# Optimization experiments

Hardware: AMD Instinct MI355X
Metric: run time of the kernel (lower is better)

The kernel has to match this reference:

```python
import jax, jax.numpy as jnp
import numpy as np

DROP_SPLITS = 2
KERNEL = 3


def setup_inputs() -> dict:
    key = jax.random.key(0)
    k1, k2, k3 = jax.random.split(key, 3)
    B, C, H, W = 32, 128, 128, 128
    Cin = C - C // DROP_SPLITS  # actual_in_channels = 64
    Cout = 128
    x = jax.random.normal(k1, (B, C, H, W), dtype=jnp.float32)
    w = jax.random.normal(k2, (Cout, Cin, KERNEL, KERNEL), dtype=jnp.float32) * 0.05
    b = jax.random.normal(k3, (Cout,), dtype=jnp.float32) * 0.05
    return {"x": x, "w": w, "b": b}


def reference(x, w, b):
    # x: [B, C, H, W]; w: [Cout, Cin, K, K]; b: [Cout]
    Cin = w.shape[1]
    ch_sum = x.sum(axis=(-2, -1))                 # [B, C] per-channel spatial sums
    idx = jnp.argsort(ch_sum, axis=1)[:, :Cin]    # [B, Cin] lowest-sum channels
    # batched gather of selected channels (replaces per-sample python loop)
    sel = jnp.take_along_axis(x, idx[:, :, None, None], axis=1)  # [B, Cin, H, W]
    pad = KERNEL // 2
    out = jax.lax.conv_general_dilated(
        sel, w,
        window_strides=(1, 1),
        padding=[(pad, pad), (pad, pad)],
        dimension_numbers=("NCHW", "OIHW", "NCHW"),
    )
    return out + b[None, :, None, None]
```

## Files before the change

### kernel.cpp

```cpp
#include <hip/hip_runtime.h>

#define B_ 32
#define C_ 128
#define HW_ 128
#define CIN_ 64
#define COUT_ 128
#define SPATIAL (HW_ * HW_)

typedef unsigned short u16;
typedef unsigned int u32;
typedef short s16x8 __attribute__((ext_vector_type(8)));
typedef float f32x16 __attribute__((ext_vector_type(16)));

__device__ __forceinline__ void split_bf16(float x, u16& hi, u16& lo) {
    u32 u = __float_as_uint(x);
    u32 rh = (u + 0x7FFFu + ((u >> 16) & 1u)) >> 16;
    float hf = __uint_as_float(rh << 16);
    float r = x - hf;
    u32 v = __float_as_uint(r);
    u32 rl = (v + 0x7FFFu + ((v >> 16) & 1u)) >> 16;
    hi = (u16)rh; lo = (u16)rl;
}

__device__ __forceinline__ u16 rnd_bf16(float x) {
    u32 u = __float_as_uint(x);
    return (u16)((u + 0x7FFFu + ((u >> 16) & 1u)) >> 16);
}

__global__ __launch_bounds__(256) void k_chansum(const float* __restrict__ x,
                                                 double* __restrict__ sums) {
    int bc = blockIdx.x;
    const float4* p4 = (const float4*)(x + (size_t)bc * SPATIAL);
    int t = threadIdx.x;
    double s = 0.0;
#pragma unroll
    for (int i = 0; i < 16; ++i) {
        float4 v = p4[t + 256 * i];
        s += (double)v.x + (double)v.y + (double)v.z + (double)v.w;
    }
#pragma unroll
    for (int off = 32; off > 0; off >>= 1) s += __shfl_down(s, off, 64);
    __shared__ double wsum[4];
    if ((t & 63) == 0) wsum[t >> 6] = s;
    __syncthreads();
    if (t == 0) sums[bc] = wsum[0] + wsum[1] + wsum[2] + wsum[3];
}

__global__ __launch_bounds__(128) void k_select(const double* __restrict__ sums,
                                                int* __restrict__ idx) {
    int b = blockIdx.x, c = threadIdx.x;
    __shared__ double s[C_];
    double my = sums[b * C_ + c];
    s[c] = my;
    __syncthreads();
    int rank = 0;
    for (int j = 0; j < C_; ++j) {
        double v = s[j];
        rank += (v < my || (v == my && j < c)) ? 1 : 0;
    }
    if (rank < CIN_) idx[b * CIN_ + rank] = c;
}

__global__ __launch_bounds__(256) void k_wprep(const float* __restrict__ w,
                                               u16* __restrict__ wf) {
    int bid = blockIdx.x;
    int hl = bid / 144, rem = bid % 144;
    int tap = rem / 16, r2 = rem % 16;
    int ks = r2 / 4, cot = r2 % 4;
    int dh = tap / 3, dw = tap % 3;
    for (int j = threadIdx.x; j < 512; j += 256) {
        int lane = j >> 3, e = j & 7;
        int co = cot * 32 + (lane & 31);
        int ci = ks * 16 + (lane >> 5) * 8 + e;
        float v = w[((co * CIN_ + ci) * 3 + dh) * 3 + dw];
        u16 h, l; split_bf16(v, h, l);
        wf[(size_t)bid * 512 + j] = hl ? l : h;
    }
}

#define ROWS 8
#define WC 32

__global__ __launch_bounds__(256, 2) void k_conv_mfma(
    const float* __restrict__ x, const u16* __restrict__ wf,
    const float* __restrict__ bias, const int* __restrict__ idx,
    float* __restrict__ out)
{
    __shared__ __align__(16) u16 tH[10 * 34 * 32];
    __shared__ int sidx[CIN_];

    const int b = blockIdx.z;
    const int h0 = blockIdx.y * ROWS;
    const int w0 = blockIdx.x * WC;
    const int t = threadIdx.x;
    const int lane = t & 63;
    const int wv = t >> 6;
    const int g  = wv & 1;
    const int rg = wv >> 1;
    const int lc = lane & 31;
    const int lk = lane >> 5;

    if (t < CIN_) sidx[t] = idx[b * CIN_ + t];

    f32x16 acc[2][4];
#pragma unroll
    for (int ct = 0; ct < 2; ++ct)
#pragma unroll
        for (int q = 0; q < 16; ++q) {
            int row = (q & 3) + 8 * (q >> 2) + 4 * lk;
            float bv = bias[g * 64 + ct * 32 + row];
#pragma unroll
            for (int rr = 0; rr < 4; ++rr) acc[ct][rr][q] = bv;
        }

    const float* xb = x + ((size_t)b << 21);

    for (int ch = 0; ch < 2; ++ch) {
        __syncthreads();
        for (int e = t; e < 4 * 10 * 34; e += 256) {
            int w_  = e % 34;
            int tmp = e / 34;
            int r   = tmp % 10;
            int s   = tmp / 10;
            int gh = h0 + r - 1, gw = w0 + w_ - 1;
            bool ok = ((unsigned)gh < (unsigned)HW_) && ((unsigned)gw < (unsigned)HW_);
            int cb = ch * 32 + s * 8;
            uint4 ph = {0, 0, 0, 0};
            if (ok) {
                int off = (gh << 7) + gw;
                float v0 = xb[((size_t)sidx[cb + 0] << 14) + off];
                float v1 = xb[((size_t)sidx[cb + 1] << 14) + off];
                float v2 = xb[((size_t)sidx[cb + 2] << 14) + off];
                float v3 = xb[((size_t)sidx[cb + 3] << 14) + off];
                float v4 = xb[((size_t)sidx[cb + 4] << 14) + off];
                float v5 = xb[((size_t)sidx[cb + 5] << 14) + off];
                float v6 = xb[((size_t)sidx[cb + 6] << 14) + off];
                float v7 = xb[((size_t)sidx[cb + 7] << 14) + off];
                ph.x = (u32)rnd_bf16(v0) | ((u32)rnd_bf16(v1) << 16);
                ph.y = (u32)rnd_bf16(v2) | ((u32)rnd_bf16(v3) << 16);
                ph.z = (u32)rnd_bf16(v4) | ((u32)rnd_bf16(v5) << 16);
                ph.w = (u32)rnd_bf16(v6) | ((u32)rnd_bf16(v7) << 16);
            }
            int slot = s ^ ((w_ >> 1) & 3);
            int si = (r * 34 + w_) * 32 + slot * 8;
            *(uint4*)&tH[si] = ph;
        }
        __syncthreads();

#pragma unroll 1
        for (int dh = 0; dh < 3; ++dh) {
#pragma unroll
            for (int dw = 0; dw < 3; ++dw) {
                int tap = dh * 3 + dw;
                int wT = lc + dw;
                int rbase = (rg * 4 + dh) * 34 + wT;
#pragma unroll
                for (int kci = 0; kci < 2; ++kci) {
                    int sw = ((kci * 2 + lk) ^ ((wT >> 1) & 3)) * 8;
                    uint4 bh[4];
#pragma unroll
                    for (int rr = 0; rr < 4; ++rr) {
                        int a = (rbase + rr * 34) * 32 + sw;
                        bh[rr] = *(const uint4*)&tH[a];
                    }
                    int ks = ch * 2 + kci;
                    const u16* pH = wf + ((size_t)(((0 * 9 + tap) * 4 + ks) * 4 + g * 2) * 64 + lane) * 8;
                    const u16* pL = wf + ((size_t)(((1 * 9 + tap) * 4 + ks) * 4 + g * 2) * 64 + lane) * 8;
#pragma unroll
                    for (int ct = 0; ct < 2; ++ct) {
                        s16x8 ah = *(const s16x8*)(pH + ct * 512);
                        s16x8 al = *(const s16x8*)(pL + ct * 512);
#pragma unroll
                        for (int rr = 0; rr < 4; ++rr) {
                            s16x8 bhv = __builtin_bit_cast(s16x8, bh[rr]);
                            acc[ct][rr] = __builtin_amdgcn_mfma_f32_32x32x16_bf16(ah, bhv, acc[ct][rr], 0, 0, 0);
                            acc[ct][rr] = __builtin_amdgcn_mfma_f32_32x32x16_bf16(al, bhv, acc[ct][rr], 0, 0, 0);
                        }
                    }
                }
            }
        }
    }

    const int orow0 = h0 + rg * 4;
    size_t ob = (((size_t)(b * COUT_ + g * 64)) << 14) + ((size_t)orow0 << 7) + w0 + lc;
#pragma unroll
    for (int ct = 0; ct < 2; ++ct)
#pragma unroll
        for (int rr = 0; rr < 4; ++rr)
#pragma unroll
            for (int q = 0; q < 16; ++q) {
                int row = (q & 3) + 8 * (q >> 2) + 4 * lk;
                out[ob + (((size_t)(ct * 32 + row)) << 14) + ((size_t)rr << 7)] = acc[ct][rr][q];
            }
}

extern "C" void kernel_launch(void* const* d_in, const int* in_sizes, int n_in,
                              void* d_out, int out_size, void* d_ws, size_t ws_size,
                              hipStream_t stream) {
    const float* x    = (const float*)d_in[0];
    const float* w    = (const float*)d_in[1];
    const float* bias = (const float*)d_in[2];
    float* out = (float*)d_out;

    double* sums = (double*)d_ws;
    int* idx     = (int*)((char*)d_ws + 32768);
    u16* wfrag   = (u16*)((char*)d_ws + 40960);

    k_chansum<<<B_ * C_, 256, 0, stream>>>(x, sums);
    k_select<<<B_, 128, 0, stream>>>(sums, idx);
    k_wprep<<<288, 256, 0, stream>>>(w, wfrag);

    dim3 grid(HW_ / WC, HW_ / ROWS, B_);
    k_conv_mfma<<<grid, 256, 0, stream>>>(x, wfrag, bias, idx, out);
}
```

Baseline: 607.8 us.

## Double-buffer 16-channel input tiles with register prefetch overlapping MFMA compute

Splits the 64 selected input channels into four 16-channel stages with two LDS buffers. The global gathers for the next stage are held in registers while MFMAs run on the current buffer, then written to LDS after a barrier. This hides global load latency behind compute, and the MFMA block also raises wave priority with s_setprio. The cost is 24 extra prefetch registers per thread on top of the large accumulator set, which may hurt occupancy or cause spills, plus more barriers.

```diff
diff --git a/kernel.cpp b/kernel.cpp
--- a/kernel.cpp
+++ b/kernel.cpp
@@ -25,6 +25,10 @@
 __device__ __forceinline__ u16 rnd_bf16(float x) {
     u32 u = __float_as_uint(x);
     return (u16)((u + 0x7FFFu + ((u >> 16) & 1u)) >> 16);
+}
+
+__device__ __forceinline__ u32 pack2(float a, float b) {
+    return (u32)rnd_bf16(a) | ((u32)rnd_bf16(b) << 16);
 }
 
 __global__ __launch_bounds__(256) void k_chansum(const float* __restrict__ x,
@@ -80,13 +84,15 @@
 
 #define ROWS 8
 #define WC 32
+#define TSZ (10 * 34 * 16)
+#define UNITS (2 * 10 * 34)
 
 __global__ __launch_bounds__(256, 2) void k_conv_mfma(
     const float* __restrict__ x, const u16* __restrict__ wf,
     const float* __restrict__ bias, const int* __restrict__ idx,
     float* __restrict__ out)
 {
-    __shared__ __align__(16) u16 tH[10 * 34 * 32];
+    __shared__ __align__(16) u16 tile[2][TSZ];
     __shared__ int sidx[CIN_];
 
     const int b = blockIdx.z;
@@ -115,70 +121,97 @@
 
     const float* xb = x + ((size_t)b << 21);
 
-    for (int ch = 0; ch < 2; ++ch) {
-        __syncthreads();
-        for (int e = t; e < 4 * 10 * 34; e += 256) {
+    float pre[3][8];
+
+    auto issue = [&](int qq) {
+#pragma unroll
+        for (int u = 0; u < 3; ++u) {
+            int e = t + 256 * u;
+            bool ve = (e < UNITS);
             int w_  = e % 34;
             int tmp = e / 34;
             int r   = tmp % 10;
             int s   = tmp / 10;
             int gh = h0 + r - 1, gw = w0 + w_ - 1;
-            bool ok = ((unsigned)gh < (unsigned)HW_) && ((unsigned)gw < (unsigned)HW_);
-            int cb = ch * 32 + s * 8;
-            uint4 ph = {0, 0, 0, 0};
-            if (ok) {
-                int off = (gh << 7) + gw;
-                float v0 = xb[((size_t)sidx[cb + 0] << 14) + off];
-                float v1 = xb[((size_t)sidx[cb + 1] << 14) + off];
-                float v2 = xb[((size_t)sidx[cb + 2] << 14) + off];
-                float v3 = xb[((size_t)sidx[cb + 3] << 14) + off];
-                float v4 = xb[((size_t)sidx[cb + 4] << 14) + off];
-                float v5 = xb[((size_t)sidx[cb + 5] << 14) + off];
-                float v6 = xb[((size_t)sidx[cb + 6] << 14) + off];
-                float v7 = xb[((size_t)sidx[cb + 7] << 14) + off];
-                ph.x = (u32)rnd_bf16(v0) | ((u32)rnd_bf16(v1) << 16);
-                ph.y = (u32)rnd_bf16(v2) | ((u32)rnd_bf16(v3) << 16);
-                ph.z = (u32)rnd_bf16(v4) | ((u32)rnd_bf16(v5) << 16);
-                ph.w = (u32)rnd_bf16(v6) | ((u32)rnd_bf16(v7) << 16);
-            }
-            int slot = s ^ ((w_ >> 1) & 3);
-            int si = (r * 34 + w_) * 32 + slot * 8;
-            *(uint4*)&tH[si] = ph;
-        }
-        __syncthreads();
-
-#pragma unroll 1
+            bool ok = ve && ((unsigned)gh < (unsigned)HW_) && ((unsigned)gw < (unsigned)HW_);
+            int off = (gh << 7) + gw;
+            int cb = qq * 16 + s * 8;
+#pragma unroll
+            for (int i = 0; i < 8; ++i) {
+                float v = 0.f;
+                if (ok) v = xb[((size_t)sidx[cb + i] << 14) + off];
+                pre[u][i] = v;
+            }
+        }
+    };
+
+    auto commit = [&](int buf) {
+#pragma unroll
+        for (int u = 0; u < 3; ++u) {
+            int e = t + 256 * u;
+            if (e < UNITS) {
+                int w_  = e % 34;
+                int tmp = e / 34;
+                int r   = tmp % 10;
+                int s   = tmp / 10;
+                uint4 ph;
+                ph.x = pack2(pre[u][0], pre[u][1]);
+                ph.y = pack2(pre[u][2], pre[u][3]);
+                ph.z = pack2(pre[u][4], pre[u][5]);
+                ph.w = pack2(pre[u][6], pre[u][7]);
+                int slot = s ^ ((w_ >> 2) & 1);
+                int si = (r * 34 + w_) * 16 + slot * 8;
+                *(uint4*)&tile[buf][si] = ph;
+            }
+        }
+    };
+
+    auto compute = [&](int qq, int buf) {
+#pragma unroll
         for (int dh = 0; dh < 3; ++dh) {
 #pragma unroll
             for (int dw = 0; dw < 3; ++dw) {
-                int tap = dh * 3 + dw;
+                const int tap = dh * 3 + dw;
                 int wT = lc + dw;
-                int rbase = (rg * 4 + dh) * 34 + wT;
-#pragma unroll
-                for (int kci = 0; kci < 2; ++kci) {
-                    int sw = ((kci * 2 + lk) ^ ((wT >> 1) & 3)) * 8;
-                    uint4 bh[4];
+                int sr = (lk ^ ((wT >> 2) & 1)) * 8;
+                uint4 bh[4];
+#pragma unroll
+                for (int rr = 0; rr < 4; ++rr) {
+                    int a = ((rg * 4 + dh + rr) * 34 + wT) * 16 + sr;
+                    bh[rr] = *(const uint4*)&tile[buf][a];
+                }
+                const u16* pH = wf + ((size_t)(((0 * 9 + tap) * 4 + qq) * 4 + g * 2) << 9) + lane * 8;
+                const u16* pL = wf + ((size_t)(((1 * 9 + tap) * 4 + qq) * 4 + g * 2) << 9) + lane * 8;
+                __builtin_amdgcn_s_setprio(1);
+#pragma unroll
+                for (int ct = 0; ct < 2; ++ct) {
+                    s16x8 ah = *(const s16x8*)(pH + ct * 512);
+                    s16x8 al = *(const s16x8*)(pL + ct * 512);
 #pragma unroll
                     for (int rr = 0; rr < 4; ++rr) {
-                        int a = (rbase + rr * 34) * 32 + sw;
-                        bh[rr] = *(const uint4*)&tH[a];
-                    }
-                    int ks = ch * 2 + kci;
-                    const u16* pH = wf + ((size_t)(((0 * 9 + tap) * 4 + ks) * 4 + g * 2) * 64 + lane) * 8;
-                    const u16* pL = wf + ((size_t)(((1 * 9 + tap) * 4 + ks) * 4 + g * 2) * 64 + lane) * 8;
-#pragma unroll
-                    for (int ct = 0; ct < 2; ++ct) {
-                        s16x8 ah = *(const s16x8*)(pH + ct * 512);
-                        s16x8 al = *(const s16x8*)(pL + ct * 512);
-#pragma unroll
-                        for (int rr = 0; rr < 4; ++rr) {
-                            s16x8 bhv = __builtin_bit_cast(s16x8, bh[rr]);
-                            acc[ct][rr] = __builtin_amdgcn_mfma_f32_32x32x16_bf16(ah, bhv, acc[ct][rr], 0, 0, 0);
-                            acc[ct][rr] = __builtin_amdgcn_mfma_f32_32x32x16_bf16(al, bhv, acc[ct][rr], 0, 0, 0);
-                        }
+                        s16x8 bv = __builtin_bit_cast(s16x8, bh[rr]);
+                        acc[ct][rr] = __builtin_amdgcn_mfma_f32_32x32x16_bf16(ah, bv, acc[ct][rr], 0, 0, 0);
+                        acc[ct][rr] = __builtin_amdgcn_mfma_f32_32x32x16_bf16(al, bv, acc[ct][rr], 0, 0, 0);
                     }
                 }
-            }
+                __builtin_amdgcn_s_setprio(0);
+            }
+        }
+    };
+
+    __syncthreads();
+    issue(0);
+    commit(0);
+    __syncthreads();
+
+#pragma unroll 1
+    for (int qq = 0; qq < 4; ++qq) {
+        if (qq < 3) issue(qq + 1);
+        compute(qq, qq & 1);
+        __syncthreads();
+        if (qq < 3) {
+            commit((qq + 1) & 1);
+            __syncthreads();
         }
     }
 
```

Measured after the change: 612.1 us. About the same (+0.7%).
